# Kernel optimization log

Measured on AMD Instinct MI355X. Metric: run time of the kernel, lower is better.

The kernel has to match this reference:

```python
import jax, jax.numpy as jnp
import numpy as np
import math

R, C, B, E = 64, 256, 1, 768
H, DK, F = 8, 96, 3072
EPS = 1e-5


def _ln(x, w, b):
    m = jnp.mean(x, axis=-1, keepdims=True)
    v = jnp.var(x, axis=-1, keepdims=True)
    return (x - m) / jnp.sqrt(v + EPS) * w + b


def _lin(x, w, b):
    # torch Linear: y = x @ W^T + b, W: [out, in]
    return jnp.einsum('...i,oi->...o', x, w) + b


def setup_inputs() -> dict:
    key = jax.random.key(0)
    ks = jax.random.split(key, 16)
    w = lambda k, s: jax.random.normal(k, s, dtype=jnp.float32) * 0.02
    z = lambda s: jnp.zeros(s, dtype=jnp.float32)
    o = lambda s: jnp.ones(s, dtype=jnp.float32)
    return {
        'x': jax.random.normal(ks[0], (R, C, B, E), dtype=jnp.float32),
        'ln_row_w': o((E,)), 'ln_row_b': z((E,)),
        'row_q_w': w(ks[1], (E, E)), 'row_q_b': z((E,)),
        'row_k_w': w(ks[2], (E, E)), 'row_k_b': z((E,)),
        'row_v_w': w(ks[3], (E, E)), 'row_v_b': z((E,)),
        'row_o_w': w(ks[4], (E, E)), 'row_o_b': z((E,)),
        'ln_col_w': o((E,)), 'ln_col_b': z((E,)),
        'col_q_w': w(ks[5], (E, E)), 'col_q_b': z((E,)),
        'col_k_w': w(ks[6], (E, E)), 'col_k_b': z((E,)),
        'col_v_w': w(ks[7], (E, E)), 'col_v_b': z((E,)),
        'col_o_w': w(ks[8], (E, E)), 'col_o_b': z((E,)),
        'ln_ffn_w': o((E,)), 'ln_ffn_b': z((E,)),
        'fc1_w': w(ks[9], (F, E)), 'fc1_b': z((F,)),
        'fc2_w': w(ks[10], (E, F)), 'fc2_b': z((E,)),
    }


def reference(x, ln_row_w, ln_row_b, row_q_w, row_q_b, row_k_w, row_k_b,
              row_v_w, row_v_b, row_o_w, row_o_b,
              ln_col_w, ln_col_b, col_q_w, col_q_b, col_k_w, col_k_b,
              col_v_w, col_v_b, col_o_w, col_o_b,
              ln_ffn_w, ln_ffn_b, fc1_w, fc1_b, fc2_w, fc2_b):
    r, c, n, e = x.shape  # n_rows, n_cols, batch, embed

    # ---- Row self-attention (pre-LN residual block) ----
    xn = _ln(x, ln_row_w, ln_row_b)
    scaling = (DK ** -0.5) / math.sqrt(r)  # align_scaling: extra 1/sqrt(n_rows)
    q = _lin(xn, row_q_w, row_q_b).reshape(r, c, n, H, DK) * scaling
    k = _lin(xn, row_k_w, row_k_b).reshape(r, c, n, H, DK)
    v = _lin(xn, row_v_w, row_v_b).reshape(r, c, n, H, DK)
    row_logits = jnp.einsum('rinhd,rjnhd->hnij', q, k)  # sums over rows
    row_probs = jax.nn.softmax(row_logits, axis=-1)     # [H, B, C, C]
    rc = jnp.einsum('hnij,rjnhd->rinhd', row_probs, v).reshape(r, c, n, e)
    x = x + _lin(rc, row_o_w, row_o_b)

    # ---- Column self-attention (pre-LN residual block) ----
    xn = _ln(x, ln_col_w, ln_col_b)
    q = _lin(xn, col_q_w, col_q_b).reshape(r, c, n, H, DK) * (DK ** -0.5)
    k = _lin(xn, col_k_w, col_k_b).reshape(r, c, n, H, DK)
    v = _lin(xn, col_v_w, col_v_b).reshape(r, c, n, H, DK)
    col_logits = jnp.einsum('icnhd,jcnhd->hcnij', q, k)
    col_probs = jax.nn.softmax(col_logits, axis=-1)     # [H, C, B, R, R]
    cc = jnp.einsum('hcnij,jcnhd->icnhd', col_probs, v).reshape(r, c, n, e)
    x = x + _lin(cc, col_o_w, col_o_b)

    # ---- Feed-forward (pre-LN residual block) ----
    xn = _ln(x, ln_ffn_w, ln_ffn_b)
    h = jax.nn.gelu(_lin(xn, fc1_w, fc1_b), approximate=False)
    x = x + _lin(h, fc2_w, fc2_b)

    return x, row_probs, col_probs
```

## Files before the change

kernel.cpp:

```cpp
#include <hip/hip_runtime.h>
#include <cstdint>

typedef unsigned short u16;
typedef __attribute__((ext_vector_type(8))) short short8;
typedef __attribute__((ext_vector_type(4))) short short4v;
typedef __attribute__((ext_vector_type(4))) float floatx4;

#define DEV __device__ __forceinline__

DEV float bf2f(u16 u) { union { uint32_t i; float f; } w; w.i = ((uint32_t)u) << 16; return w.f; }
DEV u16 f2bf(float f) {
  union { float f; uint32_t i; } w; w.f = f;
  uint32_t x = w.i;
  return (u16)((x + 0x7fffu + ((x >> 16) & 1u)) >> 16);
}

DEV float fast_gelu(float x) {
  const float y = x * 0.70710678118f;
  const float ay = fabsf(y);
  const float t = 1.f / (1.f + 0.3275911f * ay);
  const float poly = t * (0.254829592f + t * (-0.284496736f +
                     t * (1.421413741f + t * (-1.453152027f + t * 1.061405429f))));
  const float er = 1.f - poly * __expf(-y * y);
  const float erf_y = __builtin_copysignf(er, y);
  return 0.5f * x * (1.f + erf_y);
}

DEV void async_copy16(const u16* g, u16* l) {
  __builtin_amdgcn_global_load_lds(
      (const __attribute__((address_space(1))) void*)(uintptr_t)g,
      (__attribute__((address_space(3))) void*)(uint32_t)(uintptr_t)l,
      16, 0, 0);
}

struct CvtArgs {
  const float* src[10];
  float scale[10];
};
__global__ __launch_bounds__(256) void cvt_all(CvtArgs a, u16* __restrict__ dst) {
  const size_t e = ((size_t)blockIdx.x * 256 + threadIdx.x) * 4;
  if (e >= 9437184) return;
  int reg;
  size_t base;
  if (e < 4718592) { reg = (int)(e / 589824); base = (size_t)reg * 589824; }
  else if (e < 7077888) { reg = 8; base = 4718592; }
  else { reg = 9; base = 7077888; }
  const float sc = a.scale[reg];
  floatx4 f = *(const floatx4*)(a.src[reg] + (e - base));
  short4v o;
#pragma unroll
  for (int j = 0; j < 4; ++j) o[j] = (short)f2bf(f[j] * sc);
  *(short4v*)(dst + e) = o;
}

__global__ __launch_bounds__(256) void bias_pack(const float* __restrict__ qb,
                                                 const float* __restrict__ kb,
                                                 const float* __restrict__ vb,
                                                 float sq, float* __restrict__ out) {
  const int i = blockIdx.x * 256 + threadIdx.x;
  if (i >= 2304) return;
  const int buf = i / 768, c = i - buf * 768;
  out[i] = buf == 0 ? qb[c] * sq : (buf == 1 ? kb[c] : vb[c]);
}

template<bool INF32>
__global__ __launch_bounds__(256) void ln_kernel(const void* __restrict__ in,
                                                 const float* __restrict__ w,
                                                 const float* __restrict__ b,
                                                 u16* __restrict__ out) {
  const int wid = threadIdx.x >> 6, lane = threadIdx.x & 63;
  const int row = blockIdx.x * 4 + wid;
  const size_t base = (size_t)row * 768;
  float v[12];
#pragma unroll
  for (int p = 0; p < 3; ++p) {
    const int e = p * 256 + lane * 4;
    if constexpr (INF32) {
      floatx4 f = *(const floatx4*)((const float*)in + base + e);
#pragma unroll
      for (int j = 0; j < 4; ++j) v[p * 4 + j] = f[j];
    } else {
      short4v u = *(const short4v*)((const u16*)in + base + e);
#pragma unroll
      for (int j = 0; j < 4; ++j) v[p * 4 + j] = bf2f((u16)u[j]);
    }
  }
  float s = 0.f, sq = 0.f;
#pragma unroll
  for (int i = 0; i < 12; ++i) { s += v[i]; sq += v[i] * v[i]; }
#pragma unroll
  for (int m = 1; m < 64; m <<= 1) { s += __shfl_xor(s, m); sq += __shfl_xor(sq, m); }
  const float mean = s * (1.f / 768.f);
  const float var = sq * (1.f / 768.f) - mean * mean;
  const float rstd = rsqrtf(var + 1e-5f);
#pragma unroll
  for (int p = 0; p < 3; ++p) {
    const int e = p * 256 + lane * 4;
    floatx4 wv = *(const floatx4*)(w + e);
    floatx4 bv = *(const floatx4*)(b + e);
    short4v o;
#pragma unroll
    for (int j = 0; j < 4; ++j) {
      float y = (v[p * 4 + j] - mean) * rstd * wv[j] + bv[j];
      o[j] = (short)f2bf(y);
    }
    *(short4v*)(out + base + e) = o;
  }
}

template<int AMODE, int EPI>
__global__ __launch_bounds__(256) void gemm_bt(
    const u16* __restrict__ A, const u16* __restrict__ B,
    const float* __restrict__ bias, const void* __restrict__ res,
    void* __restrict__ out, int K, int lda, int ldb,
    long long aBatch, long long bBatch, long long outBatch, int ldc, float scale) {
  __shared__ u16 lA[128 * 32];
  __shared__ u16 lB[128 * 32];
  const int t = threadIdx.x;
  const int z = blockIdx.z;
  const int m0 = blockIdx.x * 128, n0 = blockIdx.y * 128;
  const u16* Ab;
  const u16* Bb;
  int koff = 0;
  if constexpr (AMODE == 0) { Ab = A + (size_t)z * aBatch; Bb = B + (size_t)z * bBatch; }
  else if constexpr (AMODE == 1) { Ab = A + z * 96; Bb = B + z * 96; }
  else { const int h = z >> 4; Ab = A + h * 96; Bb = B + h * 96; koff = (z & 15) * 384; }

  const int krow = t >> 2;
  const int kcol = (t & 3) << 3;
  const int wid = t >> 6, lane = t & 63;
  const int wr = wid >> 1, wc = wid & 1;
  const int lrow = lane & 15, lhi = lane >> 4;

  floatx4 acc[4][4];
#pragma unroll
  for (int i = 0; i < 4; ++i)
#pragma unroll
    for (int j = 0; j < 4; ++j) acc[i][j] = (floatx4){0.f, 0.f, 0.f, 0.f};

  for (int k0 = 0; k0 < K; k0 += 32) {
#pragma unroll
    for (int i = 0; i < 2; ++i) {
      const int row = i * 64 + krow;
      const int kk = koff + k0 + kcol;
      const u16 *ga, *gb;
      if constexpr (AMODE == 0) {
        ga = Ab + (size_t)(m0 + row) * lda + kk;
        gb = Bb + (size_t)(n0 + row) * ldb + kk;
      } else {
        const int r = kk / 96, d = kk - r * 96;
        ga = Ab + (size_t)r * 196608 + (size_t)(m0 + row) * 768 + d;
        gb = Bb + (size_t)r * 196608 + (size_t)(n0 + row) * 768 + d;
      }
      async_copy16(ga, lA + i * 2048 + wid * 512);
      async_copy16(gb, lB + i * 2048 + wid * 512);
    }
    asm volatile("s_waitcnt vmcnt(0)" ::: "memory");
    __syncthreads();

    short8 af[4], bfr[4];
#pragma unroll
    for (int mi = 0; mi < 4; ++mi)
      af[mi] = *(const short8*)&lA[(wr * 64 + mi * 16 + lrow) * 32 + lhi * 8];
#pragma unroll
    for (int ni = 0; ni < 4; ++ni)
      bfr[ni] = *(const short8*)&lB[(wc * 64 + ni * 16 + lrow) * 32 + lhi * 8];
#pragma unroll
    for (int mi = 0; mi < 4; ++mi)
#pragma unroll
      for (int ni = 0; ni < 4; ++ni)
        acc[mi][ni] = __builtin_amdgcn_mfma_f32_16x16x32_bf16(af[mi], bfr[ni], acc[mi][ni], 0, 0, 0);
    __syncthreads();
  }

  const int mbase = m0 + wr * 64;
  const int nbase = n0 + wc * 64;
#pragma unroll
  for (int mi = 0; mi < 4; ++mi) {
#pragma unroll
    for (int ni = 0; ni < 4; ++ni) {
      const int n = nbase + ni * 16 + lrow;
      float bz = 0.f;
      if constexpr (EPI != 1 && EPI != 7) { if (bias) bz = bias[n]; }
#pragma unroll
      for (int r4 = 0; r4 < 4; ++r4) {
        const int m = mbase + mi * 16 + lhi * 4 + r4;
        const float val = acc[mi][ni][r4];
        if constexpr (EPI == 1) {
          ((float*)out)[(size_t)z * outBatch + (size_t)m * ldc + n] = val;
        } else if constexpr (EPI == 2) {
          ((u16*)out)[(size_t)m * ldc + n] = f2bf(fast_gelu(val + bz));
        } else if constexpr (EPI == 3) {
          const float r = ((const float*)res)[(size_t)m * ldc + n];
          ((float*)out)[(size_t)m * ldc + n] = r + val + bz;
        } else if constexpr (EPI == 4) {
          const float r = ((const float*)res)[(size_t)m * ldc + n];
          ((u16*)out)[(size_t)m * ldc + n] = f2bf(r + val + bz);
        } else if constexpr (EPI == 5) {
          const float r = bf2f(((const u16*)res)[(size_t)m * ldc + n]);
          ((float*)out)[(size_t)m * ldc + n] = r + val + bz;
        } else if constexpr (EPI == 6) {
          const float r = bf2f(((const u16*)res)[(size_t)m * ldc + n]);
          ((u16*)out)[(size_t)m * ldc + n] = f2bf(r + val + bz);
        } else if constexpr (EPI == 7) {
          const int rr = n / 96, d = n - rr * 96;
          ((u16*)out)[((size_t)(rr * 256 + m)) * 768 + (size_t)z * 96 + d] = f2bf(val);
        } else if constexpr (EPI == 8) {
          const int buf = n / 768, col = n - buf * 768;
          ((u16*)out)[(size_t)buf * 12582912 + (size_t)m * 768 + col] = f2bf(val + bz);
        }
      }
    }
  }
}

__global__ __launch_bounds__(256) void softmax_row(const float* __restrict__ part,
                                                   float* __restrict__ probs_f,
                                                   u16* __restrict__ probs_b) {
  const int wid = threadIdx.x >> 6, lane = threadIdx.x & 63;
  const int row = blockIdx.x * 4 + wid;
  const int h = row >> 8, i = row & 255;
  const size_t base = (size_t)h * 16 * 65536 + (size_t)i * 256 + lane * 4;
  floatx4 v = (floatx4){0.f, 0.f, 0.f, 0.f};
#pragma unroll
  for (int s16 = 0; s16 < 16; ++s16) {
    floatx4 p = *(const floatx4*)(part + base + (size_t)s16 * 65536);
#pragma unroll
    for (int j = 0; j < 4; ++j) v[j] += p[j];
  }
  float mx = fmaxf(fmaxf(v[0], v[1]), fmaxf(v[2], v[3]));
#pragma unroll
  for (int m = 1; m < 64; m <<= 1) mx = fmaxf(mx, __shfl_xor(mx, m));
  float e[4], s = 0.f;
#pragma unroll
  for (int j = 0; j < 4; ++j) { e[j] = __expf(v[j] - mx); s += e[j]; }
#pragma unroll
  for (int m = 1; m < 64; m <<= 1) s += __shfl_xor(s, m);
  const float inv = 1.f / s;
  floatx4 of;
  short4v ob;
#pragma unroll
  for (int j = 0; j < 4; ++j) {
    const float p = e[j] * inv;
    of[j] = p;
    ob[j] = (short)f2bf(p);
  }
  *(floatx4*)(probs_f + (size_t)row * 256 + lane * 4) = of;
  *(short4v*)(probs_b + (size_t)row * 256 + lane * 4) = ob;
}

__global__ __launch_bounds__(256) void pack_vt(const u16* __restrict__ v, u16* __restrict__ vt) {
  __shared__ u16 S[64][104];
  const int jb = blockIdx.x, r = blockIdx.y, h = blockIdx.z;
  const int t = threadIdx.x;
#pragma unroll
  for (int p = 0; p < 3; ++p) {
    const int cid = t + p * 256;
    const int j = cid / 12, ch = cid - j * 12;
    short8 x = *(const short8*)&v[((size_t)(r * 256 + jb * 64 + j)) * 768 + h * 96 + ch * 8];
    *(short8*)&S[j][ch * 8] = x;
  }
  __syncthreads();
#pragma unroll
  for (int p = 0; p < 3; ++p) {
    const int cid = t + p * 256;
    const int d = cid / 8, cj = cid - d * 8;
    u16 tmp[8];
#pragma unroll
    for (int m = 0; m < 8; ++m) tmp[m] = S[cj * 8 + m][d];
    *(short8*)&vt[((size_t)(h * 6144 + r * 96 + d)) * 256 + jb * 64 + cj * 8] = *(short8*)tmp;
  }
}

__global__ __launch_bounds__(256) void col_attn(const u16* __restrict__ q,
                                                const u16* __restrict__ k,
                                                const u16* __restrict__ v,
                                                float* __restrict__ probs,
                                                u16* __restrict__ ctx) {
  __shared__ u16 qs[64][104];
  __shared__ u16 ks[64][104];
  __shared__ u16 vt[96][72];
  __shared__ u16 ps[64][72];
  const int c = blockIdx.x, h = blockIdx.y;
  const int t = threadIdx.x;
#pragma unroll
  for (int p = 0; p < 3; ++p) {
    const int cid = t + p * 256;
    const int i = cid / 12, ch = cid - i * 12;
    const size_t g = ((size_t)(i * 256 + c)) * 768 + h * 96 + ch * 8;
    short8 qv = *(const short8*)(q + g);
    short8 kv = *(const short8*)(k + g);
    short8 vv = *(const short8*)(v + g);
    *(short8*)&qs[i][ch * 8] = qv;
    *(short8*)&ks[i][ch * 8] = kv;
#pragma unroll
    for (int m = 0; m < 8; ++m) vt[ch * 8 + m][i] = (u16)vv[m];
  }
  __syncthreads();
  const int lane = t & 63, wid = t >> 6;
  const int lrow = lane & 15, lhi = lane >> 4;

  floatx4 s[4];
#pragma unroll
  for (int nj = 0; nj < 4; ++nj) s[nj] = (floatx4){0.f, 0.f, 0.f, 0.f};
#pragma unroll
  for (int kk = 0; kk < 3; ++kk) {
    short8 a = *(const short8*)&qs[wid * 16 + lrow][kk * 32 + lhi * 8];
#pragma unroll
    for (int nj = 0; nj < 4; ++nj) {
      short8 bb = *(const short8*)&ks[nj * 16 + lrow][kk * 32 + lhi * 8];
      s[nj] = __builtin_amdgcn_mfma_f32_16x16x32_bf16(a, bb, s[nj], 0, 0, 0);
    }
  }
  const size_t pb = ((size_t)(h * 256 + c)) * 4096;
#pragma unroll
  for (int r4 = 0; r4 < 4; ++r4) {
    float mx = fmaxf(fmaxf(s[0][r4], s[1][r4]), fmaxf(s[2][r4], s[3][r4]));
    mx = fmaxf(mx, __shfl_xor(mx, 1));
    mx = fmaxf(mx, __shfl_xor(mx, 2));
    mx = fmaxf(mx, __shfl_xor(mx, 4));
    mx = fmaxf(mx, __shfl_xor(mx, 8));
    float e[4], sum = 0.f;
#pragma unroll
    for (int nj = 0; nj < 4; ++nj) { e[nj] = __expf(s[nj][r4] - mx); sum += e[nj]; }
    sum += __shfl_xor(sum, 1);
    sum += __shfl_xor(sum, 2);
    sum += __shfl_xor(sum, 4);
    sum += __shfl_xor(sum, 8);
    const float inv = 1.f / sum;
    const int i = wid * 16 + lhi * 4 + r4;
#pragma unroll
    for (int nj = 0; nj < 4; ++nj) {
      const float pv = e[nj] * inv;
      const int j = nj * 16 + lrow;
      probs[pb + (size_t)i * 64 + j] = pv;
      ps[i][j] = f2bf(pv);
    }
  }
  __syncthreads();
  floatx4 o[6];
#pragma unroll
  for (int df = 0; df < 6; ++df) o[df] = (floatx4){0.f, 0.f, 0.f, 0.f};
#pragma unroll
  for (int k2 = 0; k2 < 2; ++k2) {
    short8 a = *(const short8*)&ps[wid * 16 + lrow][k2 * 32 + lhi * 8];
#pragma unroll
    for (int df = 0; df < 6; ++df) {
      short8 bb = *(const short8*)&vt[df * 16 + lrow][k2 * 32 + lhi * 8];
      o[df] = __builtin_amdgcn_mfma_f32_16x16x32_bf16(a, bb, o[df], 0, 0, 0);
    }
  }
#pragma unroll
  for (int df = 0; df < 6; ++df)
#pragma unroll
    for (int r4 = 0; r4 < 4; ++r4) {
      const int i = wid * 16 + lhi * 4 + r4;
      const int d = df * 16 + lrow;
      ctx[((size_t)(i * 256 + c)) * 768 + h * 96 + d] = f2bf(o[df][r4]);
    }
}

extern "C" void kernel_launch(void* const* d_in, const int* in_sizes, int n_in,
                              void* d_out, int out_size, void* d_ws, size_t ws_size,
                              hipStream_t stream) {
  const float* x_in  = (const float*)d_in[0];
  const float* lnr_w = (const float*)d_in[1];
  const float* lnr_b = (const float*)d_in[2];
  const float* rq_w  = (const float*)d_in[3];
  const float* rq_b  = (const float*)d_in[4];
  const float* rk_w  = (const float*)d_in[5];
  const float* rk_b  = (const float*)d_in[6];
  const float* rv_w  = (const float*)d_in[7];
  const float* rv_b  = (const float*)d_in[8];
  const float* ro_w  = (const float*)d_in[9];
  const float* ro_b  = (const float*)d_in[10];
  const float* lnc_w = (const float*)d_in[11];
  const float* lnc_b = (const float*)d_in[12];
  const float* cq_w  = (const float*)d_in[13];
  const float* cq_b  = (const float*)d_in[14];
  const float* ck_w  = (const float*)d_in[15];
  const float* ck_b  = (const float*)d_in[16];
  const float* cv_w  = (const float*)d_in[17];
  const float* cv_b  = (const float*)d_in[18];
  const float* co_w  = (const float*)d_in[19];
  const float* co_b  = (const float*)d_in[20];
  const float* lnf_w = (const float*)d_in[21];
  const float* lnf_b = (const float*)d_in[22];
  const float* f1_w  = (const float*)d_in[23];
  const float* f1_b  = (const float*)d_in[24];
  const float* f2_w  = (const float*)d_in[25];
  const float* f2_b  = (const float*)d_in[26];

  const float s_row = 0.0127577591f;
  const float s_col = 0.1020620726f;

  char* ws = (char*)d_ws;
  const size_t WSZ_E = 589824 * 2;
  u16* w_all = (u16*)ws;
  u16* w_rqkv = w_all;
  u16* w_ro   = (u16*)(ws + 3 * WSZ_E);
  u16* w_cqkv = (u16*)(ws + 4 * WSZ_E);
  u16* w_co   = (u16*)(ws + 7 * WSZ_E);
  u16* w_f1   = (u16*)(ws + 8 * WSZ_E);
  u16* w_f2   = (u16*)(ws + 8 * WSZ_E + 4718592);
  size_t off = 8 * WSZ_E + 2 * 4718592;

  const bool xf32 = ws_size >= 147849216ULL;
  char* x_cur = ws + off;
  off += xf32 ? 50331648 : 25165824;
  u16* qb = (u16*)(ws + off); off += 25165824;
  u16* kb = (u16*)(ws + off); off += 25165824;
  u16* vb = (u16*)(ws + off); off += 25165824;
  u16* probsb = (u16*)(ws + off); off += 1048576;
  float* qkvb_row = (float*)(ws + off); off += 9216;
  float* qkvb_col = (float*)(ws + off); off += 9216;

  u16* vt     = qb;
  u16* ctx1   = kb;
  u16* hidden = qb;
  u16* xn3    = vb;

  float* out_x  = (float*)d_out;
  float* out_rp = out_x + 12582912;
  float* out_cp = out_x + 13107200;
  u16* xn   = (u16*)out_x;
  u16* ctx2 = (u16*)((char*)out_x + 25165824);
  float* part = out_x;

  const dim3 blk(256);

  CvtArgs ca;
  ca.src[0] = rq_w; ca.src[1] = rk_w; ca.src[2] = rv_w; ca.src[3] = ro_w;
  ca.src[4] = cq_w; ca.src[5] = ck_w; ca.src[6] = cv_w; ca.src[7] = co_w;
  ca.src[8] = f1_w; ca.src[9] = f2_w;
  for (int i = 0; i < 10; ++i) ca.scale[i] = 1.f;
  ca.scale[0] = s_row; ca.scale[4] = s_col;
  cvt_all<<<9216, blk, 0, stream>>>(ca, w_all);
  bias_pack<<<9, blk, 0, stream>>>(rq_b, rk_b, rv_b, s_row, qkvb_row);
  bias_pack<<<9, blk, 0, stream>>>(cq_b, ck_b, cv_b, s_col, qkvb_col);

  ln_kernel<true><<<4096, blk, 0, stream>>>(x_in, lnr_w, lnr_b, xn);
  gemm_bt<0, 8><<<dim3(128, 18, 1), blk, 0, stream>>>(xn, w_rqkv, qkvb_row, nullptr, qb, 768, 768, 768, 0, 0, 0, 768, 1.f);
  gemm_bt<2, 1><<<dim3(2, 2, 128), blk, 0, stream>>>(qb, kb, nullptr, nullptr, part, 384, 0, 0, 0, 0, 65536LL, 256, 1.f);
  softmax_row<<<512, blk, 0, stream>>>(part, out_rp, probsb);
  pack_vt<<<dim3(4, 64, 8), blk, 0, stream>>>(vb, vt);
  gemm_bt<0, 7><<<dim3(2, 48, 8), blk, 0, stream>>>(probsb, vt, nullptr, nullptr, ctx1, 256, 256, 256, 65536LL, 1572864LL, 0, 0, 1.f);
  if (xf32)
    gemm_bt<0, 3><<<dim3(128, 6, 1), blk, 0, stream>>>(ctx1, w_ro, ro_b, x_in, x_cur, 768, 768, 768, 0, 0, 0, 768, 1.f);
  else
    gemm_bt<0, 4><<<dim3(128, 6, 1), blk, 0, stream>>>(ctx1, w_ro, ro_b, x_in, x_cur, 768, 768, 768, 0, 0, 0, 768, 1.f);

  if (xf32) ln_kernel<true><<<4096, blk, 0, stream>>>(x_cur, lnc_w, lnc_b, xn);
  else      ln_kernel<false><<<4096, blk, 0, stream>>>(x_cur, lnc_w, lnc_b, xn);
  gemm_bt<0, 8><<<dim3(128, 18, 1), blk, 0, stream>>>(xn, w_cqkv, qkvb_col, nullptr, qb, 768, 768, 768, 0, 0, 0, 768, 1.f);
  col_attn<<<dim3(256, 8), blk, 0, stream>>>(qb, kb, vb, out_cp, ctx2);
  if (xf32)
    gemm_bt<0, 3><<<dim3(128, 6, 1), blk, 0, stream>>>(ctx2, w_co, co_b, x_cur, x_cur, 768, 768, 768, 0, 0, 0, 768, 1.f);
  else
    gemm_bt<0, 6><<<dim3(128, 6, 1), blk, 0, stream>>>(ctx2, w_co, co_b, x_cur, x_cur, 768, 768, 768, 0, 0, 0, 768, 1.f);

  if (xf32) ln_kernel<true><<<4096, blk, 0, stream>>>(x_cur, lnf_w, lnf_b, xn3);
  else      ln_kernel<false><<<4096, blk, 0, stream>>>(x_cur, lnf_w, lnf_b, xn3);
  gemm_bt<0, 2><<<dim3(128, 12, 1), blk, 0, stream>>>(xn3, w_f1, f1_b, nullptr, hidden, 768, 768, 768, 0, 0, 0, 1536, 1.f);
  if (xf32)
    gemm_bt<0, 3><<<dim3(128, 6, 1), blk, 0, stream>>>(hidden, w_f2, f2_b, x_cur, out_x, 1536, 1536, 3072, 0, 0, 0, 768, 1.f);
  else
    gemm_bt<0, 5><<<dim3(128, 6, 1), blk, 0, stream>>>(hidden, w_f2, f2_b, x_cur, out_x, 1536, 1536, 3072, 0, 0, 0, 768, 1.f);
  gemm_bt<0, 2><<<dim3(128, 12, 1), blk, 0, stream>>>(xn3, w_f1 + 1536 * 768, f1_b + 1536, nullptr, hidden, 768, 768, 768, 0, 0, 0, 1536, 1.f);
  gemm_bt<0, 3><<<dim3(128, 6, 1), blk, 0, stream>>>(hidden, w_f2 + 1536, nullptr, out_x, out_x, 1536, 1536, 3072, 0, 0, 0, 768, 1.f);
}
```

Baseline: 662.6 us.

## Triple-buffer GEMM LDS tiles with async prefetch and XOR-swizzled reads

```diff
diff --git a/kernel.cpp b/kernel.cpp
--- a/kernel.cpp
+++ b/kernel.cpp
@@ -108,14 +108,37 @@
   }
 }
 
+template<int AMODE>
+DEV void stage_tile(const u16* __restrict__ Ab, const u16* __restrict__ Bb,
+                    int m0, int n0, int lda, int ldb, int kk0, int t,
+                    u16* ldsA, u16* ldsB) {
+  const int wid = t >> 6;
+  const int col = (((t & 3) ^ ((t >> 2) & 3)) << 3);
+#pragma unroll
+  for (int i = 0; i < 2; ++i) {
+    const int r = i * 64 + (t >> 2);
+    const int kk = kk0 + col;
+    const u16 *ga, *gb;
+    if constexpr (AMODE == 0) {
+      ga = Ab + (size_t)(m0 + r) * lda + kk;
+      gb = Bb + (size_t)(n0 + r) * ldb + kk;
+    } else {
+      const int r96 = kk / 96, d = kk - r96 * 96;
+      ga = Ab + (size_t)r96 * 196608 + (size_t)(m0 + r) * 768 + d;
+      gb = Bb + (size_t)r96 * 196608 + (size_t)(n0 + r) * 768 + d;
+    }
+    async_copy16(ga, ldsA + i * 2048 + wid * 512);
+    async_copy16(gb, ldsB + i * 2048 + wid * 512);
+  }
+}
+
 template<int AMODE, int EPI>
 __global__ __launch_bounds__(256) void gemm_bt(
     const u16* __restrict__ A, const u16* __restrict__ B,
     const float* __restrict__ bias, const void* __restrict__ res,
     void* __restrict__ out, int K, int lda, int ldb,
     long long aBatch, long long bBatch, long long outBatch, int ldc, float scale) {
-  __shared__ u16 lA[128 * 32];
-  __shared__ u16 lB[128 * 32];
+  __shared__ u16 lds[3 * 8192];
   const int t = threadIdx.x;
   const int z = blockIdx.z;
   const int m0 = blockIdx.x * 128, n0 = blockIdx.y * 128;
@@ -126,11 +149,10 @@
   else if constexpr (AMODE == 1) { Ab = A + z * 96; Bb = B + z * 96; }
   else { const int h = z >> 4; Ab = A + h * 96; Bb = B + h * 96; koff = (z & 15) * 384; }
 
-  const int krow = t >> 2;
-  const int kcol = (t & 3) << 3;
   const int wid = t >> 6, lane = t & 63;
   const int wr = wid >> 1, wc = wid & 1;
   const int lrow = lane & 15, lhi = lane >> 4;
+  const int swl = lrow & 3;
 
   floatx4 acc[4][4];
 #pragma unroll
@@ -138,39 +160,49 @@
 #pragma unroll
     for (int j = 0; j < 4; ++j) acc[i][j] = (floatx4){0.f, 0.f, 0.f, 0.f};
 
-  for (int k0 = 0; k0 < K; k0 += 32) {
-#pragma unroll
-    for (int i = 0; i < 2; ++i) {
-      const int row = i * 64 + krow;
-      const int kk = koff + k0 + kcol;
-      const u16 *ga, *gb;
-      if constexpr (AMODE == 0) {
-        ga = Ab + (size_t)(m0 + row) * lda + kk;
-        gb = Bb + (size_t)(n0 + row) * ldb + kk;
-      } else {
-        const int r = kk / 96, d = kk - r * 96;
-        ga = Ab + (size_t)r * 196608 + (size_t)(m0 + row) * 768 + d;
-        gb = Bb + (size_t)r * 196608 + (size_t)(n0 + row) * 768 + d;
-      }
-      async_copy16(ga, lA + i * 2048 + wid * 512);
-      async_copy16(gb, lB + i * 2048 + wid * 512);
-    }
-    asm volatile("s_waitcnt vmcnt(0)" ::: "memory");
-    __syncthreads();
-
+  const int NT = K >> 5;
+
+  stage_tile<AMODE>(Ab, Bb, m0, n0, lda, ldb, koff, t, lds, lds + 4096);
+  if (NT > 1)
+    stage_tile<AMODE>(Ab, Bb, m0, n0, lda, ldb, koff + 32, t, lds + 8192, lds + 8192 + 4096);
+  if (NT > 2) asm volatile("s_waitcnt vmcnt(4)" ::: "memory");
+  else        asm volatile("s_waitcnt vmcnt(0)" ::: "memory");
+  __builtin_amdgcn_s_barrier();
+  asm volatile("" ::: "memory");
+
+  int cur = 0, nxt = 2;
+  for (int kt = 0; kt < NT; ++kt) {
+    const bool more = (kt + 2) < NT;
+    if (more)
+      stage_tile<AMODE>(Ab, Bb, m0, n0, lda, ldb, koff + (kt + 2) * 32, t,
+                        lds + nxt * 8192, lds + nxt * 8192 + 4096);
+
+    const u16* lA = lds + cur * 8192;
+    const u16* lB = lA + 4096;
     short8 af[4], bfr[4];
 #pragma unroll
     for (int mi = 0; mi < 4; ++mi)
-      af[mi] = *(const short8*)&lA[(wr * 64 + mi * 16 + lrow) * 32 + lhi * 8];
+      af[mi] = *(const short8*)&lA[(wr * 64 + mi * 16 + lrow) * 32 + ((lhi ^ swl) << 3)];
 #pragma unroll
     for (int ni = 0; ni < 4; ++ni)
-      bfr[ni] = *(const short8*)&lB[(wc * 64 + ni * 16 + lrow) * 32 + lhi * 8];
+      bfr[ni] = *(const short8*)&lB[(wc * 64 + ni * 16 + lrow) * 32 + ((lhi ^ swl) << 3)];
+
+    __builtin_amdgcn_s_setprio(1);
 #pragma unroll
     for (int mi = 0; mi < 4; ++mi)
 #pragma unroll
       for (int ni = 0; ni < 4; ++ni)
         acc[mi][ni] = __builtin_amdgcn_mfma_f32_16x16x32_bf16(af[mi], bfr[ni], acc[mi][ni], 0, 0, 0);
-    __syncthreads();
+    __builtin_amdgcn_s_setprio(0);
+
+    if (kt + 1 < NT) {
+      if (more) asm volatile("s_waitcnt vmcnt(4)" ::: "memory");
+      else      asm volatile("s_waitcnt vmcnt(0)" ::: "memory");
+      __builtin_amdgcn_s_barrier();
+      asm volatile("" ::: "memory");
+    }
+    cur = (cur == 2) ? 0 : cur + 1;
+    nxt = (nxt == 2) ? 0 : nxt + 1;
   }
 
   const int mbase = m0 + wr * 64;
```

Result: faster. 620.1 us (-6.4%).
